# Optimization experiments

Measured on AMD Instinct MI355X. Metric: run time of the kernel, lower is better.

The kernel has to match this reference:

```python
import jax, jax.numpy as jnp
import numpy as np

EPS = 1e-8  # torch cosine_similarity eps


def setup_inputs() -> dict:
    key = jax.random.key(0)
    ks = jax.random.split(key, 8)
    B, D = 65536, 1024
    s = lambda fi, fo: (1.0 / np.sqrt(fi))
    return {
        "image_features": jax.random.normal(ks[0], (B, D), jnp.float32),
        "W1": jax.random.normal(ks[1], (D, 512), jnp.float32) * s(D, 512),
        "b1": jnp.zeros((512,), jnp.float32),
        "W2": jax.random.normal(ks[2], (512, 256), jnp.float32) * s(512, 256),
        "b2": jnp.zeros((256,), jnp.float32),
        "W3": jax.random.normal(ks[3], (256, 128), jnp.float32) * s(256, 128),
        "b3": jnp.zeros((128,), jnp.float32),
        "emb": jax.random.normal(ks[4], (1000, 128), jnp.float32),
    }


def reference(image_features, W1, b1, W2, b2, W3, b3, emb):
    # MLP projection (dropout is identity at inference)
    h = jax.nn.relu(image_features @ W1 + b1)
    h = jax.nn.relu(h @ W2 + b2)
    proj = h @ W3 + b3                              # [B, 128]
    # cosine similarity against all 1000 scene embeddings, fused as
    # normalize + small matmul instead of the broadcasted [B,1000,128] tensor
    pn = proj / jnp.maximum(jnp.linalg.norm(proj, axis=-1, keepdims=True), EPS)
    en = emb / jnp.maximum(jnp.linalg.norm(emb, axis=-1, keepdims=True), EPS)
    sims = pn @ en.T                                # [B, 1000]
    top_indices = jnp.argmax(sims, axis=1)          # [B]
    return top_indices
```

## Files before the change

kernel.cpp:

```cpp
#include <hip/hip_runtime.h>
#include <math.h>

#define EPS 1e-8f
#define TAU 1e-4f

typedef _Float16 half_t;
typedef __attribute__((ext_vector_type(8))) _Float16 f16x8;
typedef __attribute__((ext_vector_type(4))) float f32x4;

__device__ __forceinline__ void gload16(const half_t* g, half_t* l) {
    __builtin_amdgcn_global_load_lds((const __attribute__((address_space(1))) void*)g,
                                     (__attribute__((address_space(3))) void*)l, 16, 0, 0);
}

__device__ __forceinline__ void split2(float a, half_t& h, half_t& l) {
    h = (half_t)a;
    l = (half_t)(a - (float)h);
}

__global__ __launch_bounds__(256) void prep_kernel(
    const float* __restrict__ emb, float* __restrict__ enT,
    half_t* __restrict__ eTh, half_t* __restrict__ eTl,
    const float* __restrict__ W1, half_t* __restrict__ W1h, half_t* __restrict__ W1l,
    const float* __restrict__ W2, half_t* __restrict__ W2h, half_t* __restrict__ W2l,
    const float* __restrict__ W3, half_t* __restrict__ W3h, half_t* __restrict__ W3l,
    int* __restrict__ cnt)
{
    const int b = blockIdx.x;
    const int t = threadIdx.x;
    if (b == 0 && t == 0) *cnt = 0;
    if (b < 250) {
        const int row = b * 4 + (t >> 6);
        const int lane = t & 63;
        float e0 = emb[row * 128 + lane];
        float e1 = emb[row * 128 + 64 + lane];
        float s = e0 * e0 + e1 * e1;
#pragma unroll
        for (int off = 32; off >= 1; off >>= 1) s += __shfl_xor(s, off);
        float denom = fmaxf(sqrtf(s), EPS);
        enT[(size_t)lane * 1000 + row]        = e0 / denom;
        enT[(size_t)(64 + lane) * 1000 + row] = e1 / denom;
    } else if (b < 506) {
        const int n = (b - 250) * 4 + (t >> 6);
        const int lane = t & 63;
        float e0 = 0.f, e1 = 0.f;
        if (n < 1000) {
            e0 = emb[n * 128 + lane];
            e1 = emb[n * 128 + 64 + lane];
        }
        float s = e0 * e0 + e1 * e1;
#pragma unroll
        for (int off = 32; off >= 1; off >>= 1) s += __shfl_xor(s, off);
        float denom = fmaxf(sqrtf(s), EPS);
        float v0 = (n < 1000) ? e0 / denom : 0.f;
        float v1 = (n < 1000) ? e1 / denom : 0.f;
        half_t h, l;
        int f0 = lane, f1 = 64 + lane;
        size_t p0 = ((size_t)(f0 >> 3) * 1024 + n) * 8 + (f0 & 7);
        size_t p1 = ((size_t)(f1 >> 3) * 1024 + n) * 8 + (f1 & 7);
        split2(v0, h, l); eTh[p0] = h; eTl[p0] = l;
        split2(v1, h, l); eTh[p1] = h; eTl[p1] = l;
    } else if (b < 2554) {
        int idx = (b - 506) * 256 + t;
        int k = idx / 512, n = idx % 512;
        half_t h, l;
        split2(W1[idx], h, l);
        size_t pos = ((size_t)(k >> 3) * 512 + n) * 8 + (k & 7);
        W1h[pos] = h; W1l[pos] = l;
    } else if (b < 3066) {
        int idx = (b - 2554) * 256 + t;
        int k = idx / 256, n = idx % 256;
        half_t h, l;
        split2(W2[idx], h, l);
        size_t pos = ((size_t)(k >> 3) * 256 + n) * 8 + (k & 7);
        W2h[pos] = h; W2l[pos] = l;
    } else {
        int idx = (b - 3066) * 256 + t;
        int k = idx / 128, n = idx % 128;
        half_t h, l;
        split2(W3[idx], h, l);
        size_t pos = ((size_t)(k >> 3) * 128 + n) * 8 + (k & 7);
        W3h[pos] = h; W3l[pos] = l;
    }
}

__global__ __launch_bounds__(64) void emb_norm_kernel(const float* __restrict__ emb,
                                                      float* __restrict__ enT) {
    const int row = blockIdx.x;
    const int t = threadIdx.x;
    float e0 = emb[row * 128 + t];
    float e1 = emb[row * 128 + 64 + t];
    float s = e0 * e0 + e1 * e1;
#pragma unroll
    for (int off = 32; off >= 1; off >>= 1) s += __shfl_xor(s, off);
    float denom = fmaxf(sqrtf(s), EPS);
    enT[(size_t)t * 1000 + row]        = e0 / denom;
    enT[(size_t)(64 + t) * 1000 + row] = e1 / denom;
}

#define EPI_RELU 0
#define EPI_NORM 1

template<int K, int N, bool AF32, int EPI>
__global__ __launch_bounds__(512) void gemm16(
    const float* __restrict__ A32,
    const half_t* __restrict__ Agh, const half_t* __restrict__ Agl,
    const half_t* __restrict__ Bgh, const half_t* __restrict__ Bgl,
    const float* __restrict__ bias,
    half_t* __restrict__ Oh, half_t* __restrict__ Ol)
{
    __shared__ alignas(16) half_t sAh[2][8][128][8];
    __shared__ alignas(16) half_t sAl[2][8][128][8];
    __shared__ alignas(16) half_t sBh[2][8][128][8];
    __shared__ alignas(16) half_t sBl[2][8][128][8];

    const int t = threadIdx.x;
    const int lane = t & 63, w = t >> 6;
    const int lr = lane & 15, lg = lane >> 4;
    const int wm = w >> 1, wn = w & 1;

    const int nwg = gridDim.x * gridDim.y;
    const int lin = blockIdx.x + gridDim.x * blockIdx.y;
    const int cpx = nwg >> 3;
    const int logical = (lin & 7) * cpx + (lin >> 3);
    const int bx = logical % gridDim.x;
    const int by = logical / gridDim.x;
    const int m0 = by * 128, n0 = bx * 128;

    auto stageB = [&](int buf, int k0) {
#pragma unroll
        for (int i = 0; i < 2; ++i) {
            int s = t + 512 * i;
            int kb = s >> 7, col = s & 127;
            size_t go = ((size_t)(k0 / 8 + kb) * N + n0 + col) * 8;
            gload16(Bgh + go, &sBh[buf][0][0][0] + (size_t)s * 8);
            gload16(Bgl + go, &sBl[buf][0][0][0] + (size_t)s * 8);
        }
    };
    auto stageAf16 = [&](int buf, int k0) {
#pragma unroll
        for (int i = 0; i < 2; ++i) {
            int s = t + 512 * i;
            int kb = s >> 7, prow = s & 127;
            int row = prow ^ kb;
            size_t go = (size_t)(m0 + row) * K + k0 + kb * 8;
            gload16(Agh + go, &sAh[buf][0][0][0] + (size_t)s * 8);
            gload16(Agl + go, &sAl[buf][0][0][0] + (size_t)s * 8);
        }
    };
    float4 va0[2], va1[2];
    auto loadA32 = [&](int k0) {
#pragma unroll
        for (int q = 0; q < 2; ++q) {
            int s = t + 512 * q;
            int row = s >> 3, kb = s & 7;
            const float* src = A32 + (size_t)(m0 + row) * K + k0 + kb * 8;
            va0[q] = *(const float4*)src;
            va1[q] = *(const float4*)(src + 4);
        }
    };
    auto writeA32 = [&](int buf) {
#pragma unroll
        for (int q = 0; q < 2; ++q) {
            int s = t + 512 * q;
            int row = s >> 3, kb = s & 7;
            float vv[8] = {va0[q].x, va0[q].y, va0[q].z, va0[q].w,
                           va1[q].x, va1[q].y, va1[q].z, va1[q].w};
            f16x8 hi, lo;
#pragma unroll
            for (int i = 0; i < 8; ++i) {
                half_t h = (half_t)vv[i];
                hi[i] = h;
                lo[i] = (half_t)(vv[i] - (float)h);
            }
            int prow = row ^ kb;
            *(f16x8*)&sAh[buf][kb][prow][0] = hi;
            *(f16x8*)&sAl[buf][kb][prow][0] = lo;
        }
    };

    f32x4 acc[2][4] = {};
    constexpr int NT = K / 64;

    if constexpr (AF32) { loadA32(0); writeA32(0); }
    else stageAf16(0, 0);
    stageB(0, 0);
    __syncthreads();

    int cur = 0;
    for (int tt = 0; tt < NT; ++tt) {
        const bool hasNext = (tt + 1 < NT);
        if (hasNext) {
            const int kn = (tt + 1) * 64;
            stageB(cur ^ 1, kn);
            if constexpr (AF32) loadA32(kn);
            else stageAf16(cur ^ 1, kn);
        }
#pragma unroll
        for (int ks = 0; ks < 2; ++ks) {
            const int kb = ks * 4 + lg;
            f16x8 ah[2], al[2], bh[4], bl[4];
#pragma unroll
            for (int mf = 0; mf < 2; ++mf) {
                int row = wm * 32 + mf * 16 + lr;
                int prow = row ^ kb;
                ah[mf] = *(const f16x8*)&sAh[cur][kb][prow][0];
                al[mf] = *(const f16x8*)&sAl[cur][kb][prow][0];
            }
#pragma unroll
            for (int nf = 0; nf < 4; ++nf) {
                int col = wn * 64 + nf * 16 + lr;
                bh[nf] = *(const f16x8*)&sBh[cur][kb][col][0];
                bl[nf] = *(const f16x8*)&sBl[cur][kb][col][0];
            }
#pragma unroll
            for (int mf = 0; mf < 2; ++mf)
#pragma unroll
                for (int nf = 0; nf < 4; ++nf) {
                    acc[mf][nf] = __builtin_amdgcn_mfma_f32_16x16x32_f16(ah[mf], bh[nf], acc[mf][nf], 0, 0, 0);
                    acc[mf][nf] = __builtin_amdgcn_mfma_f32_16x16x32_f16(ah[mf], bl[nf], acc[mf][nf], 0, 0, 0);
                    acc[mf][nf] = __builtin_amdgcn_mfma_f32_16x16x32_f16(al[mf], bh[nf], acc[mf][nf], 0, 0, 0);
                }
        }
        if constexpr (AF32) { if (hasNext) writeA32(cur ^ 1); }
        __syncthreads();
        cur ^= 1;
    }

    if constexpr (EPI == EPI_RELU) {
#pragma unroll
        for (int nf = 0; nf < 4; ++nf) {
            int n = n0 + wn * 64 + nf * 16 + lr;
            float bb = bias[n];
#pragma unroll
            for (int mf = 0; mf < 2; ++mf)
#pragma unroll
                for (int r = 0; r < 4; ++r) {
                    int m = m0 + wm * 32 + mf * 16 + lg * 4 + r;
                    float v = acc[mf][nf][r] + bb;
                    v = fmaxf(v, 0.f);
                    half_t h, l;
                    split2(v, h, l);
                    Oh[(size_t)m * N + n] = h;
                    Ol[(size_t)m * N + n] = l;
                }
        }
    } else {
        __shared__ float nsum[2][128];
#pragma unroll
        for (int nf = 0; nf < 4; ++nf) {
            float bb = bias[wn * 64 + nf * 16 + lr];
#pragma unroll
            for (int mf = 0; mf < 2; ++mf)
#pragma unroll
                for (int r = 0; r < 4; ++r) acc[mf][nf][r] += bb;
        }
#pragma unroll
        for (int mf = 0; mf < 2; ++mf)
#pragma unroll
            for (int r = 0; r < 4; ++r) {
                float s = 0.f;
#pragma unroll
                for (int nf = 0; nf < 4; ++nf) {
                    float v = acc[mf][nf][r];
                    s += v * v;
                }
#pragma unroll
                for (int off = 1; off < 16; off <<= 1) s += __shfl_xor(s, off);
                if (lr == 0) nsum[wn][wm * 32 + mf * 16 + lg * 4 + r] = s;
            }
        __syncthreads();
#pragma unroll
        for (int mf = 0; mf < 2; ++mf)
#pragma unroll
            for (int r = 0; r < 4; ++r) {
                int ml = wm * 32 + mf * 16 + lg * 4 + r;
                float tot = nsum[0][ml] + nsum[1][ml];
                float sc = 1.0f / fmaxf(sqrtf(tot), EPS);
                int m = m0 + ml;
#pragma unroll
                for (int nf = 0; nf < 4; ++nf) {
                    int n = wn * 64 + nf * 16 + lr;
                    float v = acc[mf][nf][r] * sc;
                    half_t h, l;
                    split2(v, h, l);
                    Oh[(size_t)m * 128 + n] = h;
                    Ol[(size_t)m * 128 + n] = l;
                }
            }
    }
}

__global__ __launch_bounds__(256, 2) void sims64_kernel(
    const half_t* __restrict__ pnh, const half_t* __restrict__ pnl,
    const half_t* __restrict__ eTh, const half_t* __restrict__ eTl,
    int* __restrict__ out, int* __restrict__ list, int* __restrict__ cnt,
    int Mtot)
{
    __shared__ alignas(16) half_t sPnH[16 * 64 * 8];
    __shared__ alignas(16) half_t sPnL[16 * 64 * 8];
    __shared__ alignas(16) half_t sEH[16 * 64 * 8];
    __shared__ alignas(16) half_t sEL[16 * 64 * 8];
    __shared__ float sv1[128];
    __shared__ int   si1[128];
    __shared__ float sv2[128];

    const int t = threadIdx.x;
    const int lane = t & 63, w = t >> 6;
    const int lr = lane & 15, lg = lane >> 4;
    const int wm = w >> 1, wn = w & 1;
    const int m0 = blockIdx.x * 64;

#pragma unroll
    for (int i = 0; i < 4; ++i) {
        int s = t + 256 * i;
        int kb = s >> 6, row = s & 63;
        size_t go = (size_t)(m0 + row) * 128 + kb * 8;
        gload16(pnh + go, sPnH + (size_t)s * 8);
        gload16(pnl + go, sPnL + (size_t)s * 8);
    }
#pragma unroll
    for (int i = 0; i < 4; ++i) {
        int s = t + 256 * i;
        int kb = s >> 6, col = s & 63;
        size_t go = ((size_t)kb * 1024 + col) * 8;
        gload16(eTh + go, sEH + (size_t)s * 8);
        gload16(eTl + go, sEL + (size_t)s * 8);
    }

    float tv1[2][4], tv2[2][4];
    int ti1[2][4];
#pragma unroll
    for (int mf = 0; mf < 2; ++mf)
#pragma unroll
        for (int r = 0; r < 4; ++r) { tv1[mf][r] = -INFINITY; tv2[mf][r] = -INFINITY; ti1[mf][r] = 0; }

    for (int nt = 0; nt < 16; ++nt) {
        __syncthreads();
        f32x4 acc[2][2] = {};
#pragma unroll
        for (int ks = 0; ks < 4; ++ks) {
            const int kb = ks * 4 + lg;
            f16x8 ah[2], al[2], bh[2], bl[2];
#pragma unroll
            for (int mf = 0; mf < 2; ++mf) {
                int row = wm * 32 + mf * 16 + lr;
                ah[mf] = *(const f16x8*)(sPnH + ((size_t)kb * 64 + row) * 8);
                al[mf] = *(const f16x8*)(sPnL + ((size_t)kb * 64 + row) * 8);
            }
#pragma unroll
            for (int nf = 0; nf < 2; ++nf) {
                int col = wn * 32 + nf * 16 + lr;
                bh[nf] = *(const f16x8*)(sEH + ((size_t)kb * 64 + col) * 8);
                bl[nf] = *(const f16x8*)(sEL + ((size_t)kb * 64 + col) * 8);
            }
#pragma unroll
            for (int mf = 0; mf < 2; ++mf)
#pragma unroll
                for (int nf = 0; nf < 2; ++nf) {
                    acc[mf][nf] = __builtin_amdgcn_mfma_f32_16x16x32_f16(ah[mf], bh[nf], acc[mf][nf], 0, 0, 0);
                    acc[mf][nf] = __builtin_amdgcn_mfma_f32_16x16x32_f16(ah[mf], bl[nf], acc[mf][nf], 0, 0, 0);
                    acc[mf][nf] = __builtin_amdgcn_mfma_f32_16x16x32_f16(al[mf], bh[nf], acc[mf][nf], 0, 0, 0);
                }
        }
#pragma unroll
        for (int mf = 0; mf < 2; ++mf)
#pragma unroll
            for (int nf = 0; nf < 2; ++nf) {
                int gc = nt * 64 + wn * 32 + nf * 16 + lr;
#pragma unroll
                for (int r = 0; r < 4; ++r) {
                    float v = (gc < 1000) ? acc[mf][nf][r] : -INFINITY;
                    if (v > tv1[mf][r]) { tv2[mf][r] = tv1[mf][r]; tv1[mf][r] = v; ti1[mf][r] = gc; }
                    else if (v > tv2[mf][r]) tv2[mf][r] = v;
                }
            }
        __syncthreads();
        if (nt < 15) {
            int ntn = nt + 1;
#pragma unroll
            for (int i = 0; i < 4; ++i) {
                int s = t + 256 * i;
                int kb = s >> 6, col = s & 63;
                size_t go = ((size_t)kb * 1024 + ntn * 64 + col) * 8;
                gload16(eTh + go, sEH + (size_t)s * 8);
                gload16(eTl + go, sEL + (size_t)s * 8);
            }
        }
    }

#pragma unroll
    for (int mf = 0; mf < 2; ++mf)
#pragma unroll
        for (int r = 0; r < 4; ++r) {
            float v1 = tv1[mf][r], v2 = tv2[mf][r];
            int i1 = ti1[mf][r];
#pragma unroll
            for (int off = 1; off < 16; off <<= 1) {
                float ov1 = __shfl_xor(v1, off);
                int   oi1 = __shfl_xor(i1, off);
                float ov2 = __shfl_xor(v2, off);
                if (ov1 > v1) { v2 = fmaxf(v1, ov2); v1 = ov1; i1 = oi1; }
                else if (ov1 == v1) { v2 = fmaxf(v2, ov1); if (oi1 < i1) i1 = oi1; }
                else { v2 = fmaxf(v2, ov1); }
            }
            if (lr == 0) {
                int ml = wm * 32 + mf * 16 + lg * 4 + r;
                sv1[wn * 64 + ml] = v1; si1[wn * 64 + ml] = i1; sv2[wn * 64 + ml] = v2;
            }
        }
    __syncthreads();
    if (t < 64) {
        float v1 = sv1[t]; int i1 = si1[t]; float v2 = sv2[t];
        float ov1 = sv1[64 + t]; int oi1 = si1[64 + t]; float ov2 = sv2[64 + t];
        if (ov1 > v1) { v2 = fmaxf(v1, ov2); v1 = ov1; i1 = oi1; }
        else if (ov1 == v1) { v2 = fmaxf(v2, ov1); if (oi1 < i1) i1 = oi1; }
        else { v2 = fmaxf(v2, ov1); }
        out[m0 + t] = i1;
        if (v1 - v2 < TAU) {
            int p = atomicAdd(cnt, 1);
            if (p < Mtot) list[p] = m0 + t;
        }
    }
}

__global__ __launch_bounds__(256) void recheck_row_kernel(
    const float* __restrict__ img,
    const float* __restrict__ W1, const float* __restrict__ b1,
    const float* __restrict__ W2, const float* __restrict__ b2,
    const float* __restrict__ W3, const float* __restrict__ b3,
    const float* __restrict__ enT,
    const int* __restrict__ list, const int* __restrict__ count,
    int* __restrict__ out, int maxcnt)
{
    __shared__ float sx[1024];
    __shared__ float sh1[512];
    __shared__ float sh2[256];
    __shared__ float sp[128];
    __shared__ float sden;
    __shared__ float redv[4];
    __shared__ int   redi[4];

    const int t = threadIdx.x;
    const int lane = t & 63, wv = t >> 6;
    int cnt = *count;
    if (cnt > maxcnt) cnt = maxcnt;

    for (int b = blockIdx.x; b < cnt; b += gridDim.x) {
        const int row = list[b];
        *(float4*)&sx[t * 4] = *(const float4*)(img + (size_t)row * 1024 + t * 4);
        __syncthreads();
        {
            float a0 = 0.f, a1 = 0.f;
#pragma unroll 8
            for (int k = 0; k < 1024; ++k) {
                float xv = sx[k];
                float2 wv2 = *(const float2*)(W1 + (size_t)k * 512 + 2 * t);
                a0 = fmaf(xv, wv2.x, a0);
                a1 = fmaf(xv, wv2.y, a1);
            }
            sh1[2 * t]     = fmaxf(a0 + b1[2 * t], 0.f);
            sh1[2 * t + 1] = fmaxf(a1 + b1[2 * t + 1], 0.f);
        }
        __syncthreads();
        {
            float a = 0.f;
#pragma unroll 8
            for (int k = 0; k < 512; ++k)
                a = fmaf(sh1[k], W2[(size_t)k * 256 + t], a);
            sh2[t] = fmaxf(a + b2[t], 0.f);
        }
        __syncthreads();
        if (t < 128) {
            float a = 0.f;
#pragma unroll 8
            for (int k = 0; k < 256; ++k)
                a = fmaf(sh2[k], W3[(size_t)k * 128 + t], a);
            sp[t] = a + b3[t];
        }
        __syncthreads();
        if (t < 64) {
            float s = sp[t] * sp[t] + sp[t + 64] * sp[t + 64];
#pragma unroll
            for (int off = 32; off >= 1; off >>= 1) s += __shfl_xor(s, off);
            if (t == 0) sden = fmaxf(sqrtf(s), EPS);
        }
        __syncthreads();
        if (t < 128) sp[t] = sp[t] / sden;
        __syncthreads();
        float bm = -INFINITY;
        int bi = 0;
#pragma unroll
        for (int j = 0; j < 4; ++j) {
            const int c = t + 256 * j;
            if (c < 1000) {
                float a = 0.f;
#pragma unroll 8
                for (int k = 0; k < 128; ++k)
                    a = fmaf(sp[k], enT[(size_t)k * 1000 + c], a);
                if (a > bm) { bm = a; bi = c; }
            }
        }
#pragma unroll
        for (int off = 1; off < 64; off <<= 1) {
            float om = __shfl_xor(bm, off);
            int oi = __shfl_xor(bi, off);
            if (om > bm || (om == bm && oi < bi)) { bm = om; bi = oi; }
        }
        if (lane == 0) { redv[wv] = bm; redi[wv] = bi; }
        __syncthreads();
        if (t == 0) {
            float v = redv[0]; int i = redi[0];
#pragma unroll
            for (int q = 1; q < 4; ++q) {
                if (redv[q] > v || (redv[q] == v && redi[q] < i)) { v = redv[q]; i = redi[q]; }
            }
            out[row] = i;
        }
        __syncthreads();
    }
}

__global__ __launch_bounds__(256) void scene_exact_kernel(
    const float* __restrict__ img,
    const float* __restrict__ W1, const float* __restrict__ b1,
    const float* __restrict__ W2, const float* __restrict__ b2,
    const float* __restrict__ W3, const float* __restrict__ b3,
    const float* __restrict__ enT,
    int* __restrict__ out)
{
    __shared__ float sImg[16][64];
    __shared__ float sH1[16][512];
    __shared__ float sH2[16][256];
    __shared__ float sPn[16][128];

    const int tid = threadIdx.x;
    const int base = blockIdx.x * 16;

    {
        const int tx = tid & 63, ty = tid >> 6;
        float acc[4][8] = {};
        for (int k0 = 0; k0 < 1024; k0 += 64) {
            {
                const int r = tid >> 4, c4 = tid & 15;
                float4 v = *(const float4*)(img + (size_t)(base + r) * 1024 + k0 + c4 * 4);
                *(float4*)(&sImg[r][c4 * 4]) = v;
            }
            __syncthreads();
#pragma unroll 4
            for (int kk = 0; kk < 64; ++kk) {
                const int k = k0 + kk;
                float a[4];
#pragma unroll
                for (int i = 0; i < 4; ++i) a[i] = sImg[ty + 4 * i][kk];
#pragma unroll
                for (int j = 0; j < 8; ++j) {
                    float wv = W1[(size_t)k * 512 + tx + 64 * j];
#pragma unroll
                    for (int i = 0; i < 4; ++i) acc[i][j] = fmaf(a[i], wv, acc[i][j]);
                }
            }
            __syncthreads();
        }
#pragma unroll
        for (int j = 0; j < 8; ++j) {
            float bb = b1[tx + 64 * j];
#pragma unroll
            for (int i = 0; i < 4; ++i) {
                float v = acc[i][j] + bb;
                sH1[ty + 4 * i][tx + 64 * j] = v > 0.f ? v : 0.f;
            }
        }
        __syncthreads();
    }
    {
        const int tx = tid & 63, ty = tid >> 6;
        float acc[4][4] = {};
#pragma unroll 4
        for (int k = 0; k < 512; ++k) {
            float a[4];
#pragma unroll
            for (int i = 0; i < 4; ++i) a[i] = sH1[ty + 4 * i][k];
#pragma unroll
            for (int j = 0; j < 4; ++j) {
                float wv = W2[(size_t)k * 256 + tx + 64 * j];
#pragma unroll
                for (int i = 0; i < 4; ++i) acc[i][j] = fmaf(a[i], wv, acc[i][j]);
            }
        }
        __syncthreads();
#pragma unroll
        for (int j = 0; j < 4; ++j) {
            float bb = b2[tx + 64 * j];
#pragma unroll
            for (int i = 0; i < 4; ++i) {
                float v = acc[i][j] + bb;
                sH2[ty + 4 * i][tx + 64 * j] = v > 0.f ? v : 0.f;
            }
        }
        __syncthreads();
    }
    {
        const int tx = tid & 31, ty = tid >> 5;
        float acc[2][4] = {};
#pragma unroll 4
        for (int k = 0; k < 256; ++k) {
            float a[2];
#pragma unroll
            for (int i = 0; i < 2; ++i) a[i] = sH2[ty + 8 * i][k];
#pragma unroll
            for (int j = 0; j < 4; ++j) {
                float wv = W3[(size_t)k * 128 + tx + 32 * j];
#pragma unroll
                for (int i = 0; i < 2; ++i) acc[i][j] = fmaf(a[i], wv, acc[i][j]);
            }
        }
#pragma unroll
        for (int j = 0; j < 4; ++j) {
            float bb = b3[tx + 32 * j];
#pragma unroll
            for (int i = 0; i < 2; ++i) sPn[ty + 8 * i][tx + 32 * j] = acc[i][j] + bb;
        }
        __syncthreads();
    }
    {
        const int r = tid >> 4, sub = tid & 15;
        float s = 0.f;
#pragma unroll
        for (int m = 0; m < 8; ++m) {
            float v = sPn[r][sub + 16 * m];
            s += v * v;
        }
#pragma unroll
        for (int off = 1; off < 16; off <<= 1) s += __shfl_xor(s, off);
        float denom = fmaxf(sqrtf(s), EPS);
#pragma unroll
        for (int m = 0; m < 8; ++m) sPn[r][sub + 16 * m] /= denom;
        __syncthreads();
    }
    {
        const int ct = tid & 63, rg = tid >> 6;
        float bm[4]; int bi[4];
#pragma unroll
        for (int i = 0; i < 4; ++i) { bm[i] = -INFINITY; bi[i] = 0; }
#pragma unroll
        for (int tpass = 0; tpass < 2; ++tpass) {
            const int tt = ct + 64 * tpass;
            if (tt < 125) {
                const int c0 = tt * 8;
                float acc[4][8] = {};
#pragma unroll 4
                for (int k = 0; k < 128; ++k) {
                    float p[4];
#pragma unroll
                    for (int i = 0; i < 4; ++i) p[i] = sPn[rg * 4 + i][k];
                    const float* ep = enT + (size_t)k * 1000 + c0;
                    float4 e0 = *(const float4*)(ep);
                    float4 e1 = *(const float4*)(ep + 4);
                    float e[8] = {e0.x, e0.y, e0.z, e0.w, e1.x, e1.y, e1.z, e1.w};
#pragma unroll
                    for (int j = 0; j < 8; ++j)
#pragma unroll
                        for (int i = 0; i < 4; ++i) acc[i][j] = fmaf(p[i], e[j], acc[i][j]);
                }
#pragma unroll
                for (int j = 0; j < 8; ++j) {
                    const int c = c0 + j;
#pragma unroll
                    for (int i = 0; i < 4; ++i)
                        if (acc[i][j] > bm[i]) { bm[i] = acc[i][j]; bi[i] = c; }
                }
            }
        }
#pragma unroll
        for (int off = 1; off < 64; off <<= 1) {
#pragma unroll
            for (int i = 0; i < 4; ++i) {
                float om = __shfl_xor(bm[i], off);
                int oi = __shfl_xor(bi[i], off);
                if (om > bm[i] || (om == bm[i] && oi < bi[i])) { bm[i] = om; bi[i] = oi; }
            }
        }
        if (ct == 0) {
#pragma unroll
            for (int i = 0; i < 4; ++i) out[base + rg * 4 + i] = bi[i];
        }
    }
}

extern "C" void kernel_launch(void* const* d_in, const int* in_sizes, int n_in,
                              void* d_out, int out_size, void* d_ws, size_t ws_size,
                              hipStream_t stream) {
    const float* img = (const float*)d_in[0];
    const float* W1  = (const float*)d_in[1];
    const float* b1  = (const float*)d_in[2];
    const float* W2  = (const float*)d_in[3];
    const float* b2  = (const float*)d_in[4];
    const float* W3  = (const float*)d_in[5];
    const float* b3  = (const float*)d_in[6];
    const float* emb = (const float*)d_in[7];
    int* out = (int*)d_out;
    const int B = in_sizes[0] / 1024;

    size_t off = 0;
    auto carve = [&](size_t bytes) {
        void* p = (char*)d_ws + off;
        off += (bytes + 255) & ~(size_t)255;
        return p;
    };
    float*  enT  = (float*)carve(128 * 1000 * 4);
    half_t* W1h  = (half_t*)carve((size_t)1024 * 512 * 2);
    half_t* W1l  = (half_t*)carve((size_t)1024 * 512 * 2);
    half_t* W2h  = (half_t*)carve((size_t)512 * 256 * 2);
    half_t* W2l  = (half_t*)carve((size_t)512 * 256 * 2);
    half_t* W3h  = (half_t*)carve((size_t)256 * 128 * 2);
    half_t* W3l  = (half_t*)carve((size_t)256 * 128 * 2);
    half_t* eTh  = (half_t*)carve((size_t)16 * 1024 * 8 * 2);
    half_t* eTl  = (half_t*)carve((size_t)16 * 1024 * 8 * 2);
    int*    list = (int*)carve((size_t)B * 4);
    int*    cnt  = (int*)carve(256);
    half_t* h1h  = (half_t*)carve((size_t)B * 512 * 2);
    half_t* h1l  = (half_t*)carve((size_t)B * 512 * 2);
    half_t* h2h  = (half_t*)carve((size_t)B * 256 * 2);
    half_t* h2l  = (half_t*)carve((size_t)B * 256 * 2);
    const size_t REQUIRE = off;

    if (ws_size < REQUIRE) {
        emb_norm_kernel<<<1000, 64, 0, stream>>>(emb, (float*)d_ws);
        scene_exact_kernel<<<B / 16, 256, 0, stream>>>(
            img, W1, b1, W2, b2, W3, b3, (float*)d_ws, out);
        return;
    }

    half_t* pnh  = h1h;
    half_t* pnl  = (half_t*)((char*)h1h + (size_t)B * 128 * 2);

    prep_kernel<<<3194, 256, 0, stream>>>(emb, enT, eTh, eTl,
                                          W1, W1h, W1l, W2, W2h, W2l, W3, W3h, W3l,
                                          cnt);

    gemm16<1024, 512, true, EPI_RELU><<<dim3(4, B / 128), 512, 0, stream>>>(
        img, nullptr, nullptr, W1h, W1l, b1, h1h, h1l);
    gemm16<512, 256, false, EPI_RELU><<<dim3(2, B / 128), 512, 0, stream>>>(
        nullptr, h1h, h1l, W2h, W2l, b2, h2h, h2l);
    gemm16<256, 128, false, EPI_NORM><<<dim3(1, B / 128), 512, 0, stream>>>(
        nullptr, h2h, h2l, W3h, W3l, b3, pnh, pnl);

    sims64_kernel<<<B / 64, 256, 0, stream>>>(
        pnh, pnl, eTh, eTl, out, list, cnt, B);

    recheck_row_kernel<<<2048, 256, 0, stream>>>(
        img, W1, b1, W2, b2, W3, b3, enT, list, cnt, out, B);
}
```

Before: 668.7 us.

## Prefetch two K-tiles ahead with explicit waitcnt and barriers in the GEMM loop

Restructures the GEMM main loop so global loads run two K-tiles ahead instead of one. It uses explicit s_waitcnt vmcnt counts and raw s_barrier calls fenced by sched_barrier in place of __syncthreads, so async global-to-LDS loads can stay in flight across iterations. The goal is to hide global memory latency behind the MFMA work. The hand-tuned vmcnt(8) depends on exactly how many loads each stage issues, so a wrong count would silently read stale LDS data, and the extra barriers add synchronisation cost.

```diff
diff --git a/kernel.cpp b/kernel.cpp
--- a/kernel.cpp
+++ b/kernel.cpp
@@ -182,20 +182,22 @@
     f32x4 acc[2][4] = {};
     constexpr int NT = K / 64;
 
-    if constexpr (AF32) { loadA32(0); writeA32(0); }
-    else stageAf16(0, 0);
-    stageB(0, 0);
-    __syncthreads();
-
-    int cur = 0;
+    if constexpr (AF32) {
+        loadA32(0); stageB(0, 0);
+        writeA32(0);
+        loadA32(64); stageB(1, 64);
+        asm volatile("s_waitcnt vmcnt(8) lgkmcnt(0)" ::: "memory");
+    } else {
+        stageAf16(0, 0); stageB(0, 0);
+        stageAf16(1, 64); stageB(1, 64);
+        asm volatile("s_waitcnt vmcnt(8)" ::: "memory");
+    }
+    __builtin_amdgcn_sched_barrier(0);
+    __builtin_amdgcn_s_barrier();
+    __builtin_amdgcn_sched_barrier(0);
+
     for (int tt = 0; tt < NT; ++tt) {
-        const bool hasNext = (tt + 1 < NT);
-        if (hasNext) {
-            const int kn = (tt + 1) * 64;
-            stageB(cur ^ 1, kn);
-            if constexpr (AF32) loadA32(kn);
-            else stageAf16(cur ^ 1, kn);
-        }
+        const int cur = tt & 1;
 #pragma unroll
         for (int ks = 0; ks < 2; ++ks) {
             const int kb = ks * 4 + lg;
@@ -222,9 +224,32 @@
                     acc[mf][nf] = __builtin_amdgcn_mfma_f32_16x16x32_f16(al[mf], bh[nf], acc[mf][nf], 0, 0, 0);
                 }
         }
-        if constexpr (AF32) { if (hasNext) writeA32(cur ^ 1); }
-        __syncthreads();
-        cur ^= 1;
+        if (tt + 2 < NT) {
+            __builtin_amdgcn_sched_barrier(0);
+            __builtin_amdgcn_s_barrier();
+            __builtin_amdgcn_sched_barrier(0);
+            if constexpr (AF32) {
+                writeA32(cur ^ 1);
+                loadA32((tt + 2) * 64);
+                stageB(cur, (tt + 2) * 64);
+            } else {
+                stageAf16(cur, (tt + 2) * 64);
+                stageB(cur, (tt + 2) * 64);
+            }
+            asm volatile("s_waitcnt vmcnt(8) lgkmcnt(0)" ::: "memory");
+            __builtin_amdgcn_sched_barrier(0);
+            __builtin_amdgcn_s_barrier();
+            __builtin_amdgcn_sched_barrier(0);
+        } else if (tt + 1 < NT) {
+            __builtin_amdgcn_sched_barrier(0);
+            __builtin_amdgcn_s_barrier();
+            __builtin_amdgcn_sched_barrier(0);
+            if constexpr (AF32) writeA32(cur ^ 1);
+            asm volatile("s_waitcnt vmcnt(0) lgkmcnt(0)" ::: "memory");
+            __builtin_amdgcn_sched_barrier(0);
+            __builtin_amdgcn_s_barrier();
+            __builtin_amdgcn_sched_barrier(0);
+        }
     }
 
     if constexpr (EPI == EPI_RELU) {
```

Result: slower. 696.9 us (+4.2%).
